# Kernel tuning notes

Hardware: AMD Instinct MI355X
Metric: run time of the kernel (lower is better)

## Reference

```python
import jax, jax.numpy as jnp
import numpy as np

TEMPERATURE = 0.07
ASYM_F = 1.5
ASYM_M = 0.5
N_F, N_M, D = 8192, 8192, 128


def setup_inputs() -> dict:
    key = jax.random.key(0)
    kf, km = jax.random.split(key)
    proj_f = jax.random.normal(kf, (N_F, D), dtype=jnp.float32)
    proj_m = jax.random.normal(km, (N_M, D), dtype=jnp.float32)
    # module expects L2-normalized projections
    proj_f = proj_f / jnp.linalg.norm(proj_f, axis=1, keepdims=True)
    proj_m = proj_m / jnp.linalg.norm(proj_m, axis=1, keepdims=True)
    return {"proj_f": proj_f, "proj_m": proj_m}


def _directional_loss(anchor, pos, temperature):
    # anchor: (Na, D), pos: (Np, D)
    sim_pos = jnp.einsum('ad,pd->ap', anchor, pos) / temperature        # (Na, Np)
    sim_neg = jnp.einsum('ad,bd->ab', anchor, anchor) / temperature    # (Na, Na)
    n = anchor.shape[0]
    eye = jnp.eye(n, dtype=bool)
    sim_neg = jnp.where(eye, -jnp.inf, sim_neg)  # mask self-similarity
    numerator = jax.nn.logsumexp(sim_pos, axis=1)
    # logsumexp over concat([sim_pos, sim_neg]) == logaddexp of row lses (no concat materialized)
    denominator = jnp.logaddexp(numerator, jax.nn.logsumexp(sim_neg, axis=1))
    return -jnp.mean(numerator - denominator)


def reference(proj_f, proj_m):
    loss_f2m = _directional_loss(proj_f, proj_m, TEMPERATURE)
    loss_m2f = _directional_loss(proj_m, proj_f, TEMPERATURE)
    return ASYM_F * loss_f2m + ASYM_M * loss_m2f
```

## Files before the change

kernel.cpp:

```cpp
#include <hip/hip_runtime.h>

#define NROWS 8192
#define KD    128
#define K1C   20.6099291260f

typedef __bf16 bf16x8 __attribute__((ext_vector_type(8)));
typedef float  f32x4  __attribute__((ext_vector_type(4)));

typedef __attribute__((address_space(1))) void* gas_ptr;
typedef __attribute__((address_space(3))) void* las_ptr;

__device__ __forceinline__ unsigned short f2bf(float x) {
  unsigned int u = __builtin_bit_cast(unsigned int, x);
  unsigned int r = (u + 0x7FFFu + ((u >> 16) & 1u)) >> 16;
  return (unsigned short)r;
}

__global__ __launch_bounds__(256) void prep_kernel(const float4* __restrict__ F4,
                                                   const float4* __restrict__ M4,
                                                   ushort4* __restrict__ Fb4,
                                                   ushort4* __restrict__ Mb4,
                                                   float* __restrict__ sums) {
  int i = blockIdx.x * 256 + threadIdx.x;
  float4 f = F4[i];
  float4 m = M4[i];
  ushort4 fo, mo;
  fo.x = f2bf(f.x); fo.y = f2bf(f.y); fo.z = f2bf(f.z); fo.w = f2bf(f.w);
  mo.x = f2bf(m.x); mo.y = f2bf(m.y); mo.z = f2bf(m.z); mo.w = f2bf(m.w);
  Fb4[i] = fo;
  Mb4[i] = mo;
  if (i < 4 * NROWS) sums[i] = 0.0f;
}

__global__ __launch_bounds__(256, 2) void gemm_kernel(const unsigned short* __restrict__ Fb,
                                                      const unsigned short* __restrict__ Mb,
                                                      float* __restrict__ sums) {
  __shared__ __align__(16) unsigned short lds[2][128 * 128];

  const int bx = blockIdx.x;
  const int by = blockIdx.y;
  const int z  = blockIdx.z;

  const unsigned short* A;
  const unsigned short* B;
  float* rowsum;
  float* colsum = nullptr;
  if (z == 0)      { A = Fb; B = Mb; rowsum = sums;             colsum = sums + NROWS; }
  else if (z == 1) { A = Fb; B = Fb; rowsum = sums + 2 * NROWS; }
  else             { A = Mb; B = Mb; rowsum = sums + 3 * NROWS; }

  const int tid  = threadIdx.x;
  const int lane = tid & 63;
  const int wave = tid >> 6;
  const int wr = wave >> 1, wc = wave & 1;
  const int l15 = lane & 15, l4 = lane >> 4;

  auto stage = [&](unsigned short* dst, const unsigned short* src) {
    #pragma unroll
    for (int i = 0; i < 8; ++i) {
      const int c   = wave * 8 + i;
      const int lin = c * 1024 + lane * 16;
      const int row = lin >> 8;
      const int bc  = lin & 255;
      const int sbc = bc ^ ((row & 7) << 4);
      const char* s = (const char*)src + row * 256 + sbc;
      char* d = (char*)dst + c * 1024;
      __builtin_amdgcn_global_load_lds((gas_ptr)s, (las_ptr)d, 16, 0, 0);
    }
  };

  stage(lds[0], A + (size_t)by * 128 * KD);
  __syncthreads();

  bf16x8 afrag[4][4];
  #pragma unroll
  for (int m = 0; m < 4; ++m) {
    #pragma unroll
    for (int k = 0; k < 4; ++k) {
      const int row = wr * 64 + m * 16 + l15;
      const int bc  = k * 64 + l4 * 16;
      afrag[m][k] = *(const bf16x8*)((const char*)lds[0] + row * 256 + (bc ^ ((row & 7) << 4)));
    }
  }
  __syncthreads();

  float rowacc[16];
  #pragma unroll
  for (int i = 0; i < 16; ++i) rowacc[i] = 0.f;

  const unsigned short* Bbase = B + (size_t)bx * 1024 * KD;
  stage(lds[0], Bbase);
  __syncthreads();

  for (int t = 0; t < 8; ++t) {
    if (t < 7) stage(lds[(t + 1) & 1], Bbase + (size_t)(t + 1) * 128 * KD);

    f32x4 acc[4][4] = {};
    const char* bufB = (const char*)lds[t & 1];
    #pragma unroll
    for (int k = 0; k < 4; ++k) {
      bf16x8 bfrag[4];
      #pragma unroll
      for (int n = 0; n < 4; ++n) {
        const int row = wc * 64 + n * 16 + l15;
        const int bc  = k * 64 + l4 * 16;
        bfrag[n] = *(const bf16x8*)(bufB + row * 256 + (bc ^ ((row & 7) << 4)));
      }
      #pragma unroll
      for (int m = 0; m < 4; ++m)
        #pragma unroll
        for (int n = 0; n < 4; ++n)
          acc[m][n] = __builtin_amdgcn_mfma_f32_16x16x32_bf16(afrag[m][k], bfrag[n], acc[m][n], 0, 0, 0);
    }

    const bool doMask = (z > 0) && (bx * 8 + t == by);
    float colacc[4] = {0.f, 0.f, 0.f, 0.f};
    #pragma unroll
    for (int m = 0; m < 4; ++m) {
      #pragma unroll
      for (int n = 0; n < 4; ++n) {
        #pragma unroll
        for (int j = 0; j < 4; ++j) {
          float v = __builtin_amdgcn_exp2f((acc[m][n][j] - 1.0f) * K1C);
          if (doMask) {
            const int lr = wr * 64 + m * 16 + l4 * 4 + j;
            const int lc = wc * 64 + n * 16 + l15;
            if (lr == lc) v = 0.f;
          }
          rowacc[m * 4 + j] += v;
          if (z == 0) colacc[n] += v;
        }
      }
    }
    if (z == 0) {
      #pragma unroll
      for (int n = 0; n < 4; ++n) {
        float v = colacc[n];
        v += __shfl_xor(v, 16);
        v += __shfl_xor(v, 32);
        if (lane < 16)
          unsafeAtomicAdd(colsum + bx * 1024 + t * 128 + wc * 64 + n * 16 + lane, v);
      }
    }
    __syncthreads();
  }

  #pragma unroll
  for (int i = 0; i < 16; ++i) {
    float v = rowacc[i];
    v += __shfl_xor(v, 1);
    v += __shfl_xor(v, 2);
    v += __shfl_xor(v, 4);
    v += __shfl_xor(v, 8);
    rowacc[i] = v;
  }
  if (l15 == 0) {
    const int rbase = by * 128 + wr * 64 + l4 * 4;
    #pragma unroll
    for (int i = 0; i < 16; ++i)
      unsafeAtomicAdd(rowsum + rbase + (i >> 2) * 16 + (i & 3), rowacc[i]);
  }
}

__global__ __launch_bounds__(256) void loss_kernel(const float* __restrict__ sums,
                                                   float* __restrict__ out) {
  const float* Spf = sums;
  const float* Spm = sums + NROWS;
  const float* Snf = sums + 2 * NROWS;
  const float* Snm = sums + 3 * NROWS;
  float accf = 0.f, accm = 0.f;
  for (int i = threadIdx.x; i < NROWS; i += 256) {
    accf += log1pf(Snf[i] / Spf[i]);
    accm += log1pf(Snm[i] / Spm[i]);
  }
  float v = 1.5f * accf + 0.5f * accm;
  #pragma unroll
  for (int s = 1; s < 64; s <<= 1) v += __shfl_xor(v, s);
  __shared__ float red[4];
  if ((threadIdx.x & 63) == 0) red[threadIdx.x >> 6] = v;
  __syncthreads();
  if (threadIdx.x == 0) out[0] = (red[0] + red[1] + red[2] + red[3]) * (1.0f / NROWS);
}

extern "C" void kernel_launch(void* const* d_in, const int* in_sizes, int n_in,
                              void* d_out, int out_size, void* d_ws, size_t ws_size,
                              hipStream_t stream) {
  (void)in_sizes; (void)n_in; (void)out_size; (void)ws_size;
  const float* F = (const float*)d_in[0];
  const float* M = (const float*)d_in[1];
  float* out = (float*)d_out;

  float* sums = (float*)d_ws;
  unsigned short* Fb = (unsigned short*)((char*)d_ws + 4 * NROWS * sizeof(float));
  unsigned short* Mb = Fb + (size_t)NROWS * KD;

  prep_kernel<<<dim3(NROWS * KD / 4 / 256), dim3(256), 0, stream>>>(
      (const float4*)F, (const float4*)M, (ushort4*)Fb, (ushort4*)Mb, sums);
  gemm_kernel<<<dim3(8, 64, 3), dim3(256), 0, stream>>>(Fb, Mb, sums);
  loss_kernel<<<dim3(1), dim3(256), 0, stream>>>(sums, out);
}
```

Before: 101.5 us.

## Switch GEMM to 32x32x16 MFMA with 8 waves per block

The similarity GEMM moves from 16x16x32 to 32x32x16 bf16 MFMA. Block size goes from 4 to 8 waves, each wave now owning a 32x64 output tile, which cuts per-wave register pressure and is meant to raise occupancy and MFMA efficiency. A and the first B tile are staged together, and the A tile's LDS buffer is reused for B double-buffering. The exp/mask epilogue is rewritten for the new accumulator layout, and the loss reduction kernel uses 1024 threads. This risks layout-mapping mistakes in the mask and row/column reductions, and adds more atomics from extra waves.

```diff
diff --git a/kernel.cpp b/kernel.cpp
--- a/kernel.cpp
+++ b/kernel.cpp
@@ -5,7 +5,7 @@
 #define K1C   20.6099291260f
 
 typedef __bf16 bf16x8 __attribute__((ext_vector_type(8)));
-typedef float  f32x4  __attribute__((ext_vector_type(4)));
+typedef float  f32x16 __attribute__((ext_vector_type(16)));
 
 typedef __attribute__((address_space(1))) void* gas_ptr;
 typedef __attribute__((address_space(3))) void* las_ptr;
@@ -32,7 +32,7 @@
   if (i < 4 * NROWS) sums[i] = 0.0f;
 }
 
-__global__ __launch_bounds__(256, 2) void gemm_kernel(const unsigned short* __restrict__ Fb,
+__global__ __launch_bounds__(512, 4) void gemm_kernel(const unsigned short* __restrict__ Fb,
                                                       const unsigned short* __restrict__ Mb,
                                                       float* __restrict__ sums) {
   __shared__ __align__(16) unsigned short lds[2][128 * 128];
@@ -52,94 +52,94 @@
   const int tid  = threadIdx.x;
   const int lane = tid & 63;
   const int wave = tid >> 6;
-  const int wr = wave >> 1, wc = wave & 1;
-  const int l15 = lane & 15, l4 = lane >> 4;
-
-  auto stage = [&](unsigned short* dst, const unsigned short* src) {
-    #pragma unroll
-    for (int i = 0; i < 8; ++i) {
-      const int c   = wave * 8 + i;
-      const int lin = c * 1024 + lane * 16;
-      const int row = lin >> 8;
-      const int bc  = lin & 255;
-      const int sbc = bc ^ ((row & 7) << 4);
-      const char* s = (const char*)src + row * 256 + sbc;
-      char* d = (char*)dst + c * 1024;
-      __builtin_amdgcn_global_load_lds((gas_ptr)s, (las_ptr)d, 16, 0, 0);
-    }
-  };
-
-  stage(lds[0], A + (size_t)by * 128 * KD);
+  const int wr = wave >> 1;
+  const int wc = wave & 1;
+  const int l31 = lane & 31, lh = lane >> 5;
+
+  const int srow = tid >> 4;
+  const int soff = srow * 256 + ((((tid & 15) * 16)) ^ ((srow & 7) << 4));
+
+#define STAGE(dstbuf, src) do {                                                          \
+    const char* s_ = (const char*)(src) + soff;                                          \
+    char* d_ = (char*)(dstbuf) + tid * 16;                                               \
+    __builtin_amdgcn_global_load_lds((gas_ptr)(s_),         (las_ptr)(d_),         16, 0, 0); \
+    __builtin_amdgcn_global_load_lds((gas_ptr)(s_ + 8192),  (las_ptr)(d_ + 8192),  16, 0, 0); \
+    __builtin_amdgcn_global_load_lds((gas_ptr)(s_ + 16384), (las_ptr)(d_ + 16384), 16, 0, 0); \
+    __builtin_amdgcn_global_load_lds((gas_ptr)(s_ + 24576), (las_ptr)(d_ + 24576), 16, 0, 0); \
+  } while (0)
+
+  const unsigned short* Abase = A + (size_t)by * 128 * KD;
+  const unsigned short* Bbase = B + (size_t)bx * 1024 * KD;
+
+  STAGE(lds[0], Abase);
+  STAGE(lds[1], Bbase);
   __syncthreads();
 
-  bf16x8 afrag[4][4];
-  #pragma unroll
-  for (int m = 0; m < 4; ++m) {
-    #pragma unroll
-    for (int k = 0; k < 4; ++k) {
-      const int row = wr * 64 + m * 16 + l15;
-      const int bc  = k * 64 + l4 * 16;
-      afrag[m][k] = *(const bf16x8*)((const char*)lds[0] + row * 256 + (bc ^ ((row & 7) << 4)));
-    }
-  }
-  __syncthreads();
+  bf16x8 afrag[8];
+  {
+    const int arow = wr * 32 + l31;
+    const char* ab = (const char*)lds[0] + arow * 256;
+    const int sw = (arow & 7) << 4;
+    #pragma unroll
+    for (int ks = 0; ks < 8; ++ks)
+      afrag[ks] = *(const bf16x8*)(ab + ((ks * 32 + lh * 16) ^ sw));
+  }
 
   float rowacc[16];
   #pragma unroll
   for (int i = 0; i < 16; ++i) rowacc[i] = 0.f;
 
-  const unsigned short* Bbase = B + (size_t)bx * 1024 * KD;
-  stage(lds[0], Bbase);
   __syncthreads();
 
+  const int brow = wc * 64 + l31;
+  const int bsw  = (brow & 7) << 4;
+
   for (int t = 0; t < 8; ++t) {
-    if (t < 7) stage(lds[(t + 1) & 1], Bbase + (size_t)(t + 1) * 128 * KD);
-
-    f32x4 acc[4][4] = {};
-    const char* bufB = (const char*)lds[t & 1];
-    #pragma unroll
-    for (int k = 0; k < 4; ++k) {
-      bf16x8 bfrag[4];
+    if (t < 7) STAGE(lds[t & 1], Bbase + (size_t)(t + 1) * 128 * KD);
+
+    const char* bb = (const char*)lds[(t + 1) & 1];
+    const char* bb0 = bb + brow * 256;
+    const char* bb1 = bb0 + 32 * 256;
+
+    f32x16 acc0 = {}, acc1 = {};
+    #pragma unroll
+    for (int ks = 0; ks < 8; ++ks) {
+      const int c = (ks * 32 + lh * 16);
+      bf16x8 b0 = *(const bf16x8*)(bb0 + (c ^ bsw));
+      bf16x8 b1 = *(const bf16x8*)(bb1 + (c ^ bsw));
+      acc0 = __builtin_amdgcn_mfma_f32_32x32x16_bf16(afrag[ks], b0, acc0, 0, 0, 0);
+      acc1 = __builtin_amdgcn_mfma_f32_32x32x16_bf16(afrag[ks], b1, acc1, 0, 0, 0);
+    }
+
+    const bool diag = (z > 0) && (bx * 8 + t == by);
+    if (z == 0) {
+      float col0 = 0.f, col1 = 0.f;
       #pragma unroll
-      for (int n = 0; n < 4; ++n) {
-        const int row = wc * 64 + n * 16 + l15;
-        const int bc  = k * 64 + l4 * 16;
-        bfrag[n] = *(const bf16x8*)(bufB + row * 256 + (bc ^ ((row & 7) << 4)));
+      for (int r = 0; r < 16; ++r) {
+        float v0 = __builtin_amdgcn_exp2f(acc0[r] * K1C - K1C);
+        float v1 = __builtin_amdgcn_exp2f(acc1[r] * K1C - K1C);
+        rowacc[r] += v0 + v1;
+        col0 += v0; col1 += v1;
       }
+      col0 += __shfl_xor(col0, 32);
+      col1 += __shfl_xor(col1, 32);
+      if (lh == 0) {
+        float* cp = colsum + bx * 1024 + t * 128 + wc * 64 + l31;
+        unsafeAtomicAdd(cp, col0);
+        unsafeAtomicAdd(cp + 32, col1);
+      }
+    } else {
       #pragma unroll
-      for (int m = 0; m < 4; ++m)
-        #pragma unroll
-        for (int n = 0; n < 4; ++n)
-          acc[m][n] = __builtin_amdgcn_mfma_f32_16x16x32_bf16(afrag[m][k], bfrag[n], acc[m][n], 0, 0, 0);
-    }
-
-    const bool doMask = (z > 0) && (bx * 8 + t == by);
-    float colacc[4] = {0.f, 0.f, 0.f, 0.f};
-    #pragma unroll
-    for (int m = 0; m < 4; ++m) {
-      #pragma unroll
-      for (int n = 0; n < 4; ++n) {
-        #pragma unroll
-        for (int j = 0; j < 4; ++j) {
-          float v = __builtin_amdgcn_exp2f((acc[m][n][j] - 1.0f) * K1C);
-          if (doMask) {
-            const int lr = wr * 64 + m * 16 + l4 * 4 + j;
-            const int lc = wc * 64 + n * 16 + l15;
-            if (lr == lc) v = 0.f;
-          }
-          rowacc[m * 4 + j] += v;
-          if (z == 0) colacc[n] += v;
+      for (int r = 0; r < 16; ++r) {
+        float v0 = __builtin_amdgcn_exp2f(acc0[r] * K1C - K1C);
+        float v1 = __builtin_amdgcn_exp2f(acc1[r] * K1C - K1C);
+        if (diag) {
+          const int lr = wr * 32 + (r & 3) + 8 * (r >> 2) + 4 * lh;
+          const int lc = wc * 64 + l31;
+          if (lr == lc)      v0 = 0.f;
+          if (lr == lc + 32) v1 = 0.f;
         }
-      }
-    }
-    if (z == 0) {
-      #pragma unroll
-      for (int n = 0; n < 4; ++n) {
-        float v = colacc[n];
-        v += __shfl_xor(v, 16);
-        v += __shfl_xor(v, 32);
-        if (lane < 16)
-          unsafeAtomicAdd(colsum + bx * 1024 + t * 128 + wc * 64 + n * 16 + lane, v);
+        rowacc[r] += v0 + v1;
       }
     }
     __syncthreads();
@@ -152,34 +152,41 @@
     v += __shfl_xor(v, 2);
     v += __shfl_xor(v, 4);
     v += __shfl_xor(v, 8);
+    v += __shfl_xor(v, 16);
     rowacc[i] = v;
   }
-  if (l15 == 0) {
-    const int rbase = by * 128 + wr * 64 + l4 * 4;
+  if (l31 == 0) {
+    const int rbase = by * 128 + wr * 32 + 4 * lh;
     #pragma unroll
     for (int i = 0; i < 16; ++i)
-      unsafeAtomicAdd(rowsum + rbase + (i >> 2) * 16 + (i & 3), rowacc[i]);
-  }
-}
-
-__global__ __launch_bounds__(256) void loss_kernel(const float* __restrict__ sums,
-                                                   float* __restrict__ out) {
+      unsafeAtomicAdd(rowsum + rbase + (i & 3) + 8 * (i >> 2), rowacc[i]);
+  }
+#undef STAGE
+}
+
+__global__ __launch_bounds__(1024) void loss_kernel(const float* __restrict__ sums,
+                                                    float* __restrict__ out) {
   const float* Spf = sums;
   const float* Spm = sums + NROWS;
   const float* Snf = sums + 2 * NROWS;
   const float* Snm = sums + 3 * NROWS;
   float accf = 0.f, accm = 0.f;
-  for (int i = threadIdx.x; i < NROWS; i += 256) {
+  for (int i = threadIdx.x; i < NROWS; i += 1024) {
     accf += log1pf(Snf[i] / Spf[i]);
     accm += log1pf(Snm[i] / Spm[i]);
   }
   float v = 1.5f * accf + 0.5f * accm;
   #pragma unroll
   for (int s = 1; s < 64; s <<= 1) v += __shfl_xor(v, s);
-  __shared__ float red[4];
+  __shared__ float red[16];
   if ((threadIdx.x & 63) == 0) red[threadIdx.x >> 6] = v;
   __syncthreads();
-  if (threadIdx.x == 0) out[0] = (red[0] + red[1] + red[2] + red[3]) * (1.0f / NROWS);
+  if (threadIdx.x == 0) {
+    float s = 0.f;
+    #pragma unroll
+    for (int i = 0; i < 16; ++i) s += red[i];
+    out[0] = s * (1.0f / NROWS);
+  }
 }
 
 extern "C" void kernel_launch(void* const* d_in, const int* in_sizes, int n_in,
@@ -196,6 +203,6 @@
 
   prep_kernel<<<dim3(NROWS * KD / 4 / 256), dim3(256), 0, stream>>>(
       (const float4*)F, (const float4*)M, (ushort4*)Fb, (ushort4*)Mb, sums);
-  gemm_kernel<<<dim3(8, 64, 3), dim3(256), 0, stream>>>(Fb, Mb, sums);
-  loss_kernel<<<dim3(1), dim3(256), 0, stream>>>(sums, out);
-}
+  gemm_kernel<<<dim3(8, 64, 3), dim3(512), 0, stream>>>(Fb, Mb, sums);
+  loss_kernel<<<dim3(1), dim3(1024), 0, stream>>>(sums, out);
+}
```

New measurement: 100.5 us. About the same (-1.0%).

## Fold temperature scale into bf16 inputs, shrink B tiles and raise occupancy

Applied to the files above, without the earlier changes.

Pre-scales both inputs by sqrt(log2e/T) before the bf16 conversion, so the epilogue becomes a bare exp2 with no subtract or multiply. The B tile is halved to 64 rows (LDS per block halves), the per-wave accumulators shrink, and launch bounds go up to 4 blocks per CU, with the prefetch moved after the barrier and setprio wrapped around the MFMA loop. The loss kernel also uses 1024 threads. The risks are more column atomics for the f-m block, bf16 rounding now applied to the scaled values, and dropping the -1 max shift, which could overflow if dot products exceed roughly 6.

```diff
diff --git a/kernel.cpp b/kernel.cpp
--- a/kernel.cpp
+++ b/kernel.cpp
@@ -2,7 +2,7 @@
 
 #define NROWS 8192
 #define KD    128
-#define K1C   20.6099291260f
+#define SQK1C 4.5398163f
 
 typedef __bf16 bf16x8 __attribute__((ext_vector_type(8)));
 typedef float  f32x4  __attribute__((ext_vector_type(4)));
@@ -25,17 +25,19 @@
   float4 f = F4[i];
   float4 m = M4[i];
   ushort4 fo, mo;
-  fo.x = f2bf(f.x); fo.y = f2bf(f.y); fo.z = f2bf(f.z); fo.w = f2bf(f.w);
-  mo.x = f2bf(m.x); mo.y = f2bf(m.y); mo.z = f2bf(m.z); mo.w = f2bf(m.w);
+  fo.x = f2bf(f.x * SQK1C); fo.y = f2bf(f.y * SQK1C);
+  fo.z = f2bf(f.z * SQK1C); fo.w = f2bf(f.w * SQK1C);
+  mo.x = f2bf(m.x * SQK1C); mo.y = f2bf(m.y * SQK1C);
+  mo.z = f2bf(m.z * SQK1C); mo.w = f2bf(m.w * SQK1C);
   Fb4[i] = fo;
   Mb4[i] = mo;
   if (i < 4 * NROWS) sums[i] = 0.0f;
 }
 
-__global__ __launch_bounds__(256, 2) void gemm_kernel(const unsigned short* __restrict__ Fb,
+__global__ __launch_bounds__(256, 4) void gemm_kernel(const unsigned short* __restrict__ Fb,
                                                       const unsigned short* __restrict__ Mb,
                                                       float* __restrict__ sums) {
-  __shared__ __align__(16) unsigned short lds[2][128 * 128];
+  __shared__ __align__(16) unsigned short lds[2][64 * KD];
 
   const int bx = blockIdx.x;
   const int by = blockIdx.y;
@@ -55,94 +57,114 @@
   const int wr = wave >> 1, wc = wave & 1;
   const int l15 = lane & 15, l4 = lane >> 4;
 
-  auto stage = [&](unsigned short* dst, const unsigned short* src) {
+  auto stageB = [&](void* dst, const unsigned short* src) {
+    #pragma unroll
+    for (int i = 0; i < 4; ++i) {
+      const int lin = tid * 16 + i * 4096;
+      const int row = lin >> 8;
+      const int sbc = (lin & 255) ^ ((row & 7) << 4);
+      __builtin_amdgcn_global_load_lds((gas_ptr)((const char*)src + row * 256 + sbc),
+                                       (las_ptr)((char*)dst + lin), 16, 0, 0);
+    }
+  };
+
+  {
+    const unsigned short* Abase = A + (size_t)by * 128 * KD;
     #pragma unroll
     for (int i = 0; i < 8; ++i) {
-      const int c   = wave * 8 + i;
-      const int lin = c * 1024 + lane * 16;
+      const int lin = tid * 16 + i * 4096;
       const int row = lin >> 8;
-      const int bc  = lin & 255;
-      const int sbc = bc ^ ((row & 7) << 4);
-      const char* s = (const char*)src + row * 256 + sbc;
-      char* d = (char*)dst + c * 1024;
-      __builtin_amdgcn_global_load_lds((gas_ptr)s, (las_ptr)d, 16, 0, 0);
-    }
-  };
-
-  stage(lds[0], A + (size_t)by * 128 * KD);
-  __syncthreads();
-
-  bf16x8 afrag[4][4];
+      const int sbc = (lin & 255) ^ ((row & 7) << 4);
+      __builtin_amdgcn_global_load_lds((gas_ptr)((const char*)Abase + row * 256 + sbc),
+                                       (las_ptr)((char*)lds + lin), 16, 0, 0);
+    }
+  }
+  __syncthreads();
+
+  bf16x8 af[4][4];
   #pragma unroll
   for (int m = 0; m < 4; ++m) {
+    const int row = wr * 64 + m * 16 + l15;
+    const char* ab = (const char*)lds + row * 256;
+    const int sw = (row & 7) << 4;
+    #pragma unroll
+    for (int k = 0; k < 4; ++k)
+      af[m][k] = *(const bf16x8*)(ab + ((k * 64 + l4 * 16) ^ sw));
+  }
+  __syncthreads();
+
+  float rowacc[16];
+  #pragma unroll
+  for (int i = 0; i < 16; ++i) rowacc[i] = 0.f;
+
+  const unsigned short* Bbase = B + (size_t)bx * 1024 * KD;
+  stageB(lds[0], Bbase);
+  stageB(lds[1], Bbase + 64 * KD);
+  __syncthreads();
+
+  const int brow0 = wc * 32 + l15;
+  const int bsw   = (brow0 & 7) << 4;
+
+  for (int t = 0; t < 16; ++t) {
+    const char* bb = (const char*)lds[t & 1];
+    const char* pb0 = bb + brow0 * 256;
+
+    f32x4 acc[4][2] = {};
+    __builtin_amdgcn_s_setprio(1);
     #pragma unroll
     for (int k = 0; k < 4; ++k) {
-      const int row = wr * 64 + m * 16 + l15;
-      const int bc  = k * 64 + l4 * 16;
-      afrag[m][k] = *(const bf16x8*)((const char*)lds[0] + row * 256 + (bc ^ ((row & 7) << 4)));
-    }
-  }
-  __syncthreads();
-
-  float rowacc[16];
-  #pragma unroll
-  for (int i = 0; i < 16; ++i) rowacc[i] = 0.f;
-
-  const unsigned short* Bbase = B + (size_t)bx * 1024 * KD;
-  stage(lds[0], Bbase);
-  __syncthreads();
-
-  for (int t = 0; t < 8; ++t) {
-    if (t < 7) stage(lds[(t + 1) & 1], Bbase + (size_t)(t + 1) * 128 * KD);
-
-    f32x4 acc[4][4] = {};
-    const char* bufB = (const char*)lds[t & 1];
-    #pragma unroll
-    for (int k = 0; k < 4; ++k) {
-      bf16x8 bfrag[4];
+      const int c = (k * 64 + l4 * 16) ^ bsw;
+      bf16x8 b0 = *(const bf16x8*)(pb0 + c);
+      bf16x8 b1 = *(const bf16x8*)(pb0 + 16 * 256 + c);
       #pragma unroll
-      for (int n = 0; n < 4; ++n) {
-        const int row = wc * 64 + n * 16 + l15;
-        const int bc  = k * 64 + l4 * 16;
-        bfrag[n] = *(const bf16x8*)(bufB + row * 256 + (bc ^ ((row & 7) << 4)));
-      }
+      for (int m = 0; m < 4; ++m) {
+        acc[m][0] = __builtin_amdgcn_mfma_f32_16x16x32_bf16(af[m][k], b0, acc[m][0], 0, 0, 0);
+        acc[m][1] = __builtin_amdgcn_mfma_f32_16x16x32_bf16(af[m][k], b1, acc[m][1], 0, 0, 0);
+      }
+    }
+    __builtin_amdgcn_s_setprio(0);
+
+    const bool diag = (z > 0) && ((((bx << 4) + t) >> 1) == by);
+    if (z == 0) {
+      float ca0 = 0.f, ca1 = 0.f;
       #pragma unroll
-      for (int m = 0; m < 4; ++m)
-        #pragma unroll
-        for (int n = 0; n < 4; ++n)
-          acc[m][n] = __builtin_amdgcn_mfma_f32_16x16x32_bf16(afrag[m][k], bfrag[n], acc[m][n], 0, 0, 0);
-    }
-
-    const bool doMask = (z > 0) && (bx * 8 + t == by);
-    float colacc[4] = {0.f, 0.f, 0.f, 0.f};
-    #pragma unroll
-    for (int m = 0; m < 4; ++m) {
-      #pragma unroll
-      for (int n = 0; n < 4; ++n) {
+      for (int m = 0; m < 4; ++m) {
         #pragma unroll
         for (int j = 0; j < 4; ++j) {
-          float v = __builtin_amdgcn_exp2f((acc[m][n][j] - 1.0f) * K1C);
-          if (doMask) {
-            const int lr = wr * 64 + m * 16 + l4 * 4 + j;
-            const int lc = wc * 64 + n * 16 + l15;
-            if (lr == lc) v = 0.f;
+          float v0 = __builtin_amdgcn_exp2f(acc[m][0][j]);
+          float v1 = __builtin_amdgcn_exp2f(acc[m][1][j]);
+          rowacc[m * 4 + j] += v0 + v1;
+          ca0 += v0; ca1 += v1;
+        }
+      }
+      ca0 += __shfl_xor(ca0, 16);
+      ca0 += __shfl_xor(ca0, 32);
+      ca1 += __shfl_xor(ca1, 16);
+      ca1 += __shfl_xor(ca1, 32);
+      if (l4 == 0) {
+        float* cp = colsum + bx * 1024 + t * 64 + wc * 32 + l15;
+        unsafeAtomicAdd(cp, ca0);
+        unsafeAtomicAdd(cp + 16, ca1);
+      }
+    } else {
+      #pragma unroll
+      for (int m = 0; m < 4; ++m) {
+        #pragma unroll
+        for (int j = 0; j < 4; ++j) {
+          float v0 = __builtin_amdgcn_exp2f(acc[m][0][j]);
+          float v1 = __builtin_amdgcn_exp2f(acc[m][1][j]);
+          if (diag) {
+            const int grow = by * 128 + wr * 64 + m * 16 + l4 * 4 + j;
+            const int gcol = bx * 1024 + t * 64 + wc * 32 + l15;
+            if (grow == gcol)      v0 = 0.f;
+            if (grow == gcol + 16) v1 = 0.f;
           }
-          rowacc[m * 4 + j] += v;
-          if (z == 0) colacc[n] += v;
+          rowacc[m * 4 + j] += v0 + v1;
         }
       }
     }
-    if (z == 0) {
-      #pragma unroll
-      for (int n = 0; n < 4; ++n) {
-        float v = colacc[n];
-        v += __shfl_xor(v, 16);
-        v += __shfl_xor(v, 32);
-        if (lane < 16)
-          unsafeAtomicAdd(colsum + bx * 1024 + t * 128 + wc * 64 + n * 16 + lane, v);
-      }
-    }
     __syncthreads();
+    if (t < 14) stageB(lds[t & 1], Bbase + (size_t)(t + 2) * 64 * KD);
   }
 
   #pragma unroll
@@ -162,24 +184,29 @@
   }
 }
 
-__global__ __launch_bounds__(256) void loss_kernel(const float* __restrict__ sums,
-                                                   float* __restrict__ out) {
+__global__ __launch_bounds__(1024) void loss_kernel(const float* __restrict__ sums,
+                                                    float* __restrict__ out) {
   const float* Spf = sums;
   const float* Spm = sums + NROWS;
   const float* Snf = sums + 2 * NROWS;
   const float* Snm = sums + 3 * NROWS;
   float accf = 0.f, accm = 0.f;
-  for (int i = threadIdx.x; i < NROWS; i += 256) {
+  for (int i = threadIdx.x; i < NROWS; i += 1024) {
     accf += log1pf(Snf[i] / Spf[i]);
     accm += log1pf(Snm[i] / Spm[i]);
   }
   float v = 1.5f * accf + 0.5f * accm;
   #pragma unroll
   for (int s = 1; s < 64; s <<= 1) v += __shfl_xor(v, s);
-  __shared__ float red[4];
+  __shared__ float red[16];
   if ((threadIdx.x & 63) == 0) red[threadIdx.x >> 6] = v;
   __syncthreads();
-  if (threadIdx.x == 0) out[0] = (red[0] + red[1] + red[2] + red[3]) * (1.0f / NROWS);
+  if (threadIdx.x == 0) {
+    float s = 0.f;
+    #pragma unroll
+    for (int i = 0; i < 16; ++i) s += red[i];
+    out[0] = s * (1.0f / NROWS);
+  }
 }
 
 extern "C" void kernel_launch(void* const* d_in, const int* in_sizes, int n_in,
@@ -197,5 +224,5 @@
   prep_kernel<<<dim3(NROWS * KD / 4 / 256), dim3(256), 0, stream>>>(
       (const float4*)F, (const float4*)M, (ushort4*)Fb, (ushort4*)Mb, sums);
   gemm_kernel<<<dim3(8, 64, 3), dim3(256), 0, stream>>>(Fb, Mb, sums);
-  loss_kernel<<<dim3(1), dim3(256), 0, stream>>>(sums, out);
-}
+  loss_kernel<<<dim3(1), dim3(1024), 0, stream>>>(sums, out);
+}
```

After: 151.6 us. 49.3% more time.
